# Performance work log

Measured on AMD Instinct MI355X. Metric: run time of the kernel, lower is better.

## Reference

```python
import jax, jax.numpy as jnp
from jax import lax
import numpy as np

SEQ, BATCH, IN, H = 512, 256, 180, 8


def _lstm_layer(x, w_ih, w_hh, b_ih, b_hh):
    # x: [S, B, I]; PyTorch gate order: i, f, g, o stacked along 4H
    S, B, _ = x.shape
    Hh = w_hh.shape[1]
    # input contribution for all timesteps at once (one big GEMM)
    xg = jnp.einsum('sbi,gi->sbg', x, w_ih) + b_ih + b_hh  # [S, B, 4H]

    def step(carry, xt):
        h, c = carry
        g = xt + h @ w_hh.T  # [B, 4H]
        i, f, gg, o = jnp.split(g, 4, axis=-1)
        i = jax.nn.sigmoid(i)
        f = jax.nn.sigmoid(f)
        gg = jnp.tanh(gg)
        o = jax.nn.sigmoid(o)
        c = f * c + i * gg
        h = o * jnp.tanh(c)
        return (h, c), h

    init = (jnp.zeros((B, Hh), x.dtype), jnp.zeros((B, Hh), x.dtype))
    _, ys = lax.scan(step, init, xg)
    return ys  # [S, B, H]


def setup_inputs() -> dict:
    key = jax.random.key(0)
    ks = jax.random.split(key, 11)
    s = 1.0 / np.sqrt(H)  # PyTorch LSTM init scale
    return {
        'x': jax.random.normal(ks[0], (SEQ, BATCH, IN), jnp.float32),
        'w_ih0': jax.random.uniform(ks[1], (4 * H, IN), jnp.float32, -s, s),
        'w_hh0': jax.random.uniform(ks[2], (4 * H, H), jnp.float32, -s, s),
        'b_ih0': jax.random.uniform(ks[3], (4 * H,), jnp.float32, -s, s),
        'b_hh0': jax.random.uniform(ks[4], (4 * H,), jnp.float32, -s, s),
        'w_ih1': jax.random.uniform(ks[5], (4 * H, H), jnp.float32, -s, s),
        'w_hh1': jax.random.uniform(ks[6], (4 * H, H), jnp.float32, -s, s),
        'b_ih1': jax.random.uniform(ks[7], (4 * H,), jnp.float32, -s, s),
        'b_hh1': jax.random.uniform(ks[8], (4 * H,), jnp.float32, -s, s),
        'w_reg': jax.random.uniform(ks[9], (2, H), jnp.float32, -s, s),
        'b_reg': jax.random.uniform(ks[10], (2,), jnp.float32, -s, s),
    }


def reference(x, w_ih0, w_hh0, b_ih0, b_hh0, w_ih1, w_hh1, b_ih1, b_hh1, w_reg, b_reg):
    h1 = _lstm_layer(x, w_ih0, w_hh0, b_ih0, b_hh0)   # [S, B, H]
    h2 = _lstm_layer(h1, w_ih1, w_hh1, b_ih1, b_hh1)  # [S, B, H]
    S, B, Hh = h2.shape
    flat = h2.reshape(S * B, Hh)
    return flat @ w_reg.T + b_reg  # [S*B, 2]
```

## Files before the change

kernel.cpp:

```cpp
#include <hip/hip_runtime.h>

#define S_  512
#define B_  256
#define NIN 180

typedef float v2 __attribute__((ext_vector_type(2)));

#define SSIG  -1.4426950408889634f
#define STANH -2.8853900817779268f

#define QP_X1 0xB1
#define QP_X2 0x4E
#define QP_X3 0x1B
#define ROR4  0x124
#define ROR8  0x128

template<int CTRL>
__device__ __forceinline__ float dppf(float x) {
    return __uint_as_float((unsigned)__builtin_amdgcn_update_dpp(
        0, (int)__float_as_uint(x), CTRL, 0xF, 0xF, true));
}

#define ROTS8(h, r) do { \
    r[0] = (h); \
    r[1] = dppf<QP_X1>(h); \
    r[2] = dppf<QP_X2>(h); \
    r[3] = dppf<QP_X3>(h); \
    r[4] = dppf<ROR4>(h); \
    r[5] = dppf<QP_X1>(r[4]); \
    r[6] = dppf<QP_X2>(r[4]); \
    r[7] = dppf<QP_X3>(r[4]); \
} while (0)

__global__ __launch_bounds__(512) void xg_gemm(
    const float* __restrict__ x, const float* __restrict__ w,
    const float* __restrict__ bi, const float* __restrict__ bh,
    float* __restrict__ xg2)
{
    __shared__ float xs[64 * 180];

    const int tid = threadIdx.x;
    const int s   = blockIdx.x >> 2;
    const int rq  = blockIdx.x & 3;
    const int b0  = rq * 64;

    const float* xsrc = x + ((size_t)s * B_ + b0) * NIN;
    #pragma unroll
    for (int k = 0; k < 6; ++k) {
        int f4 = tid + k * 512;
        if (f4 < 2880) {
            float4 v = *(const float4*)(xsrc + 4 * (size_t)f4);
            *(float4*)&xs[4 * f4] = v;
        }
    }
    __syncthreads();

    const int wv   = __builtin_amdgcn_readfirstlane(tid >> 6);
    const int qb   = wv & 1;
    const int j0   = (wv >> 1) * 2;
    const int lane = tid & 63;
    const int b    = b0 + lane;

    const int gA0 = qb * 8 + j0;
    const int gB0 = (2 + qb) * 8 + j0;
    const float* wA0 = w + (size_t)gA0 * NIN;
    const float* wA1 = wA0 + NIN;
    const float* wB0 = w + (size_t)gB0 * NIN;
    const float* wB1 = wB0 + NIN;
    const float* xrow_ = &xs[lane * NIN];

    float a0 = 0.f, a1 = 0.f, a2 = 0.f, a3 = 0.f;
    #pragma unroll 9
    for (int ii = 0; ii < 45; ++ii) {
        float4 xv = *(const float4*)(xrow_ + 4 * ii);
        float4 wa = *(const float4*)(wA0 + 4 * ii);
        float4 wb = *(const float4*)(wB0 + 4 * ii);
        float4 wc = *(const float4*)(wA1 + 4 * ii);
        float4 wd = *(const float4*)(wB1 + 4 * ii);
        a0 = __builtin_fmaf(wa.x, xv.x, a0); a0 = __builtin_fmaf(wa.y, xv.y, a0);
        a0 = __builtin_fmaf(wa.z, xv.z, a0); a0 = __builtin_fmaf(wa.w, xv.w, a0);
        a1 = __builtin_fmaf(wb.x, xv.x, a1); a1 = __builtin_fmaf(wb.y, xv.y, a1);
        a1 = __builtin_fmaf(wb.z, xv.z, a1); a1 = __builtin_fmaf(wb.w, xv.w, a1);
        a2 = __builtin_fmaf(wc.x, xv.x, a2); a2 = __builtin_fmaf(wc.y, xv.y, a2);
        a2 = __builtin_fmaf(wc.z, xv.z, a2); a2 = __builtin_fmaf(wc.w, xv.w, a2);
        a3 = __builtin_fmaf(wd.x, xv.x, a3); a3 = __builtin_fmaf(wd.y, xv.y, a3);
        a3 = __builtin_fmaf(wd.z, xv.z, a3); a3 = __builtin_fmaf(wd.w, xv.w, a3);
    }

    const float scB = (qb == 0) ? STANH : SSIG;
    float bA0 = bi[gA0] + bh[gA0];
    float bA1 = bi[gA0 + 1] + bh[gA0 + 1];
    float bB0 = bi[gB0] + bh[gB0];
    float bB1 = bi[gB0 + 1] + bh[gB0 + 1];
    float4 o;
    o.x = SSIG * (a0 + bA0);
    o.y = scB  * (a1 + bB0);
    o.z = SSIG * (a2 + bA1);
    o.w = scB  * (a3 + bB1);
    float* dst = xg2 + (((size_t)s * 64 + (b >> 2)) * 64
                        + (b & 3) * 16 + qb * 8 + j0) * 2;
    *(float4*)dst = o;
}

__global__ __launch_bounds__(256, 1) void lstm_scan(
    const float* __restrict__ xg,
    const float* __restrict__ w_hh0,
    const float* __restrict__ w_ih1, const float* __restrict__ w_hh1,
    const float* __restrict__ b_ih1, const float* __restrict__ b_hh1,
    const float* __restrict__ w_reg, const float* __restrict__ b_reg,
    float* __restrict__ out)
{
    __shared__ float ring0[16][64];
    __shared__ float ring1[16][128];
    __shared__ float ring2[16][64];

    const int tid = threadIdx.x;
    const int wid = tid >> 6;
    const int lt  = tid & 63;
    const int j   = lt & 7;
    const int b3  = (lt >> 3) & 1;
    const int cc  = lt >> 4;
    const bool b3z = (b3 == 0);
    const int bid = blockIdx.x;

    const int gA = b3 * 8 + j;
    const int gB = (2 + b3) * 8 + j;
    const float sB_ = b3z ? STANH : SSIG;
    const float aB  = b3z ? 2.0f : 1.0f;
    const float bB  = b3z ? -1.0f : 0.0f;

    auto COMBINE2 = [&](float tA, float tB, float& c, float& h) {
        float m  = tA * tB;
        float mr = dppf<ROR8>(m);
        float fa = dppf<ROR8>(tA);
        float ob = dppf<ROR8>(tB);
        float ig = b3z ? m  : mr;
        float f  = b3z ? fa : tA;
        float o  = b3z ? ob : tB;
        c = __builtin_fmaf(f, c, ig);
        float th = __builtin_fmaf(2.0f, __builtin_amdgcn_rcpf(
            1.0f + __builtin_amdgcn_exp2f(STANH * c)), -1.0f);
        h = o * th;
    };

    if (wid == 0) {
        v2 w0p[8];
        #pragma unroll
        for (int m = 0; m < 8; ++m) {
            int k = j ^ m;
            w0p[m] = v2{SSIG * w_hh0[gA * 8 + k], sB_ * w_hh0[gB * 8 + k]};
        }
        float h0p = 0.f, c0v = 0.f;

        const float* xbase = xg + (size_t)bid * 128 + lt * 2;
        v2 xq[8];
        #pragma unroll
        for (int k = 0; k < 8; ++k) xq[k] = *(const v2*)(xbase + (size_t)k * 8192);

        for (int hh = 0; hh < 64; ++hh) {
            const float* pre = xbase + (size_t)((8 * hh + 8) & 511) * 8192;
            const int sb8 = (hh & 1) * 8;
            #pragma unroll
            for (int k = 0; k < 8; ++k) {
                v2 xc = xq[k];
                xq[k] = *(const v2*)(pre + (size_t)k * 8192);
                float r0[8];
                ROTS8(h0p, r0);
                v2 a0L = __builtin_elementwise_fma(w0p[0], v2{r0[0], r0[0]}, xc);
                v2 a0H = w0p[4] * v2{r0[4], r0[4]};
                #pragma unroll
                for (int m = 1; m < 4; ++m) {
                    a0L = __builtin_elementwise_fma(w0p[m], v2{r0[m], r0[m]}, a0L);
                    a0H = __builtin_elementwise_fma(w0p[m + 4], v2{r0[m + 4], r0[m + 4]}, a0H);
                }
                v2 a0 = a0L + a0H;
                float eA = __builtin_amdgcn_exp2f(a0.x);
                float eB = __builtin_amdgcn_exp2f(a0.y);
                float tA = __builtin_amdgcn_rcpf(1.0f + eA);
                float tB = __builtin_fmaf(aB, __builtin_amdgcn_rcpf(1.0f + eB), bB);
                COMBINE2(tA, tB, c0v, h0p);
                ring0[sb8 + k][lt] = h0p;
                if (k == 3 || k == 7) __syncthreads();
            }
        }
        __syncthreads();
        __syncthreads();
    } else if (wid == 1) {
        v2 wi1p[8];
        #pragma unroll
        for (int m = 0; m < 8; ++m) {
            int k = j ^ m;
            wi1p[m] = v2{SSIG * w_ih1[gA * 8 + k], sB_ * w_ih1[gB * 8 + k]};
        }
        const v2 b1p = v2{SSIG * (b_ih1[gA] + b_hh1[gA]),
                          sB_  * (b_ih1[gB] + b_hh1[gB])};

        __syncthreads();
        for (int p = 1; p <= 128; ++p) {
            const int sb = ((p - 1) & 3) * 4;
            float h0v[4];
            #pragma unroll
            for (int k = 0; k < 4; ++k) h0v[k] = ring0[sb + k][lt];
            #pragma unroll
            for (int k = 0; k < 4; ++k) {
                float r0[8];
                ROTS8(h0v[k], r0);
                v2 a = __builtin_elementwise_fma(wi1p[0], v2{r0[0], r0[0]}, b1p);
                #pragma unroll
                for (int m = 1; m < 8; ++m)
                    a = __builtin_elementwise_fma(wi1p[m], v2{r0[m], r0[m]}, a);
                *(v2*)&ring1[sb + k][lt * 2] = a;
            }
            __syncthreads();
        }
        __syncthreads();
    } else if (wid == 2) {
        v2 wh1p[8];
        #pragma unroll
        for (int m = 0; m < 8; ++m) {
            int k = j ^ m;
            wh1p[m] = v2{SSIG * w_hh1[gA * 8 + k], sB_ * w_hh1[gB * 8 + k]};
        }
        float h1p = 0.f, c1v = 0.f;

        auto BODY4 = [&](int p) {
            const int sb = ((p - 2) & 3) * 4;
            v2 a1in[4];
            #pragma unroll
            for (int k = 0; k < 4; ++k) a1in[k] = *(const v2*)&ring1[sb + k][lt * 2];
            #pragma unroll
            for (int k = 0; k < 4; ++k) {
                float r1[8];
                ROTS8(h1p, r1);
                v2 aL = __builtin_elementwise_fma(wh1p[0], v2{r1[0], r1[0]}, a1in[k]);
                v2 aH = wh1p[4] * v2{r1[4], r1[4]};
                #pragma unroll
                for (int m = 1; m < 4; ++m) {
                    aL = __builtin_elementwise_fma(wh1p[m], v2{r1[m], r1[m]}, aL);
                    aH = __builtin_elementwise_fma(wh1p[m + 4], v2{r1[m + 4], r1[m + 4]}, aH);
                }
                v2 a1 = aL + aH;
                float eA = __builtin_amdgcn_exp2f(a1.x);
                float eB = __builtin_amdgcn_exp2f(a1.y);
                float tA = __builtin_amdgcn_rcpf(1.0f + eA);
                float tB = __builtin_fmaf(aB, __builtin_amdgcn_rcpf(1.0f + eB), bB);
                COMBINE2(tA, tB, c1v, h1p);
                ring2[sb + k][lt] = h1p;
            }
        };

        __syncthreads();
        __syncthreads();
        for (int p = 2; p <= 128; ++p) { BODY4(p); __syncthreads(); }
        BODY4(129);
        __syncthreads();
    } else {
        float wrl[8];
        #pragma unroll
        for (int m = 0; m < 8; ++m) wrl[m] = w_reg[b3 * 8 + (j ^ m)];
        const float br  = b_reg[b3];
        const bool isl  = (j == 0);
        const int  ooff = (bid * 4 + cc) * 2 + b3;

        auto PBODY = [&](int sb, int wbase) {
            float h1v[4];
            #pragma unroll
            for (int k = 0; k < 4; ++k) h1v[k] = ring2[sb + k][lt];
            #pragma unroll
            for (int k = 0; k < 4; ++k) {
                float r1[8];
                ROTS8(h1v[k], r1);
                float pp = br;
                #pragma unroll
                for (int m = 0; m < 8; ++m) pp = __builtin_fmaf(wrl[m], r1[m], pp);
                if (isl) out[(size_t)(wbase + k) * 512 + ooff] = pp;
            }
        };

        __syncthreads();
        __syncthreads();
        __syncthreads();
        for (int p = 3; p <= 129; ++p) {
            PBODY(((p - 3) & 3) * 4, 4 * (p - 3));
            __syncthreads();
        }
        PBODY(12, 508);
    }
}

extern "C" void kernel_launch(void* const* d_in, const int* in_sizes, int n_in,
                              void* d_out, int out_size, void* d_ws, size_t ws_size,
                              hipStream_t stream) {
    (void)in_sizes; (void)n_in; (void)out_size; (void)ws_size;
    const float* x     = (const float*)d_in[0];
    const float* w_ih0 = (const float*)d_in[1];
    const float* w_hh0 = (const float*)d_in[2];
    const float* b_ih0 = (const float*)d_in[3];
    const float* b_hh0 = (const float*)d_in[4];
    const float* w_ih1 = (const float*)d_in[5];
    const float* w_hh1 = (const float*)d_in[6];
    const float* b_ih1 = (const float*)d_in[7];
    const float* b_hh1 = (const float*)d_in[8];
    const float* w_reg = (const float*)d_in[9];
    const float* b_reg = (const float*)d_in[10];
    float* out = (float*)d_out;
    float* xg2 = (float*)d_ws;

    xg_gemm<<<2048, 512, 0, stream>>>(x, w_ih0, b_ih0, b_hh0, xg2);
    lstm_scan<<<64, 256, 0, stream>>>(xg2, w_hh0, w_ih1, w_hh1, b_ih1, b_hh1,
                                      w_reg, b_reg, out);
}
```

Before: 114.5 us.

## Raise per-thread output tile in xg_gemm to reuse LDS x loads

Restructures the input-projection GEMM so each 128-thread block uses two waves-per-gate-octet layout where every thread accumulates 16 gate outputs instead of 4. Each x vector read from shared memory is reused across 16 weight rows, cutting LDS traffic and load instructions per FMA. It trades fewer waves per block and higher register usage for better arithmetic intensity; the recurrent scan kernel is unchanged.

```diff
diff --git a/kernel.cpp b/kernel.cpp
--- a/kernel.cpp
+++ b/kernel.cpp
@@ -32,7 +32,7 @@
     r[7] = dppf<QP_X3>(r[4]); \
 } while (0)
 
-__global__ __launch_bounds__(512) void xg_gemm(
+__global__ __launch_bounds__(128) void xg_gemm(
     const float* __restrict__ x, const float* __restrict__ w,
     const float* __restrict__ bi, const float* __restrict__ bh,
     float* __restrict__ xg2)
@@ -42,64 +42,62 @@
     const int tid = threadIdx.x;
     const int s   = blockIdx.x >> 2;
     const int rq  = blockIdx.x & 3;
-    const int b0  = rq * 64;
-
-    const float* xsrc = x + ((size_t)s * B_ + b0) * NIN;
+
+    const float* xsrc = x + ((size_t)s * B_ + rq * 64) * NIN;
     #pragma unroll
-    for (int k = 0; k < 6; ++k) {
-        int f4 = tid + k * 512;
-        if (f4 < 2880) {
-            float4 v = *(const float4*)(xsrc + 4 * (size_t)f4);
-            *(float4*)&xs[4 * f4] = v;
-        }
+    for (int k = 0; k < 23; ++k) {
+        int f4 = tid + k * 128;
+        if (f4 < 2880)
+            *(float4*)&xs[4 * f4] = *(const float4*)(xsrc + 4 * (size_t)f4);
     }
     __syncthreads();
 
-    const int wv   = __builtin_amdgcn_readfirstlane(tid >> 6);
-    const int qb   = wv & 1;
-    const int j0   = (wv >> 1) * 2;
+    const int oct  = __builtin_amdgcn_readfirstlane(tid >> 6);
     const int lane = tid & 63;
-    const int b    = b0 + lane;
-
-    const int gA0 = qb * 8 + j0;
-    const int gB0 = (2 + qb) * 8 + j0;
-    const float* wA0 = w + (size_t)gA0 * NIN;
-    const float* wA1 = wA0 + NIN;
-    const float* wB0 = w + (size_t)gB0 * NIN;
-    const float* wB1 = wB0 + NIN;
+    const int b    = rq * 64 + lane;
+    const float scHi = (oct == 0) ? STANH : SSIG;
+
+    float accL[8], accH[8];
+    #pragma unroll
+    for (int pp = 0; pp < 8; ++pp) { accL[pp] = 0.f; accH[pp] = 0.f; }
+
     const float* xrow_ = &xs[lane * NIN];
-
-    float a0 = 0.f, a1 = 0.f, a2 = 0.f, a3 = 0.f;
-    #pragma unroll 9
+    const float* wLo = w + (size_t)(oct * 8) * NIN;
+    const float* wHi = wLo + (size_t)16 * NIN;
+
+    #pragma unroll 3
     for (int ii = 0; ii < 45; ++ii) {
         float4 xv = *(const float4*)(xrow_ + 4 * ii);
-        float4 wa = *(const float4*)(wA0 + 4 * ii);
-        float4 wb = *(const float4*)(wB0 + 4 * ii);
-        float4 wc = *(const float4*)(wA1 + 4 * ii);
-        float4 wd = *(const float4*)(wB1 + 4 * ii);
-        a0 = __builtin_fmaf(wa.x, xv.x, a0); a0 = __builtin_fmaf(wa.y, xv.y, a0);
-        a0 = __builtin_fmaf(wa.z, xv.z, a0); a0 = __builtin_fmaf(wa.w, xv.w, a0);
-        a1 = __builtin_fmaf(wb.x, xv.x, a1); a1 = __builtin_fmaf(wb.y, xv.y, a1);
-        a1 = __builtin_fmaf(wb.z, xv.z, a1); a1 = __builtin_fmaf(wb.w, xv.w, a1);
-        a2 = __builtin_fmaf(wc.x, xv.x, a2); a2 = __builtin_fmaf(wc.y, xv.y, a2);
-        a2 = __builtin_fmaf(wc.z, xv.z, a2); a2 = __builtin_fmaf(wc.w, xv.w, a2);
-        a3 = __builtin_fmaf(wd.x, xv.x, a3); a3 = __builtin_fmaf(wd.y, xv.y, a3);
-        a3 = __builtin_fmaf(wd.z, xv.z, a3); a3 = __builtin_fmaf(wd.w, xv.w, a3);
-    }
-
-    const float scB = (qb == 0) ? STANH : SSIG;
-    float bA0 = bi[gA0] + bh[gA0];
-    float bA1 = bi[gA0 + 1] + bh[gA0 + 1];
-    float bB0 = bi[gB0] + bh[gB0];
-    float bB1 = bi[gB0 + 1] + bh[gB0 + 1];
-    float4 o;
-    o.x = SSIG * (a0 + bA0);
-    o.y = scB  * (a1 + bB0);
-    o.z = SSIG * (a2 + bA1);
-    o.w = scB  * (a3 + bB1);
-    float* dst = xg2 + (((size_t)s * 64 + (b >> 2)) * 64
-                        + (b & 3) * 16 + qb * 8 + j0) * 2;
-    *(float4*)dst = o;
+        #pragma unroll
+        for (int pp = 0; pp < 8; ++pp) {
+            float4 wa = *(const float4*)(wLo + (size_t)pp * NIN + 4 * ii);
+            float4 wb = *(const float4*)(wHi + (size_t)pp * NIN + 4 * ii);
+            accL[pp] = __builtin_fmaf(wa.x, xv.x, accL[pp]);
+            accL[pp] = __builtin_fmaf(wa.y, xv.y, accL[pp]);
+            accL[pp] = __builtin_fmaf(wa.z, xv.z, accL[pp]);
+            accL[pp] = __builtin_fmaf(wa.w, xv.w, accL[pp]);
+            accH[pp] = __builtin_fmaf(wb.x, xv.x, accH[pp]);
+            accH[pp] = __builtin_fmaf(wb.y, xv.y, accH[pp]);
+            accH[pp] = __builtin_fmaf(wb.z, xv.z, accH[pp]);
+            accH[pp] = __builtin_fmaf(wb.w, xv.w, accH[pp]);
+        }
+    }
+
+    float ob[16];
+    #pragma unroll
+    for (int pp = 0; pp < 8; ++pp) {
+        int gLo = oct * 8 + pp;
+        int gHi = gLo + 16;
+        ob[2 * pp]     = SSIG * (accL[pp] + bi[gLo] + bh[gLo]);
+        ob[2 * pp + 1] = scHi * (accH[pp] + bi[gHi] + bh[gHi]);
+    }
+    size_t base_row = ((size_t)s * 64 + (b >> 2)) * 64 + (b & 3) * 16;
+    float* dst = xg2 + (base_row + oct * 8) * 2;
+    #pragma unroll
+    for (int k = 0; k < 4; ++k) {
+        float4 o = {ob[4 * k], ob[4 * k + 1], ob[4 * k + 2], ob[4 * k + 3]};
+        *(float4*)(dst + 4 * k) = o;
+    }
 }
 
 __global__ __launch_bounds__(256, 1) void lstm_scan(
@@ -306,7 +304,7 @@
     float* out = (float*)d_out;
     float* xg2 = (float*)d_ws;
 
-    xg_gemm<<<2048, 512, 0, stream>>>(x, w_ih0, b_ih0, b_hh0, xg2);
+    xg_gemm<<<2048, 128, 0, stream>>>(x, w_ih0, b_ih0, b_hh0, xg2);
     lstm_scan<<<64, 256, 0, stream>>>(xg2, w_hh0, w_ih1, w_hh1, b_ih1, b_hh1,
                                       w_reg, b_reg, out);
 }
```

After: 175.5 us. +53.3%, slower.
